# Optimization experiments

Measured on AMD Instinct MI355X. Metric: run time of the kernel, lower is better.

Reference implementation:

```python
import jax, jax.numpy as jnp
import numpy as np

N, E, G = 16384, 65536, 64
IN_F, HID, MID, NCLS = 63, 2048, 1024, 18
EPS = 1e-5
SLOPE = 0.01  # default leaky_relu negative_slope


def setup_inputs() -> dict:
    key = jax.random.key(0)
    ks = jax.random.split(key, 24)
    p = lambda k, shp: jax.random.normal(k, shp, dtype=jnp.float32) * 0.02
    inp = {
        "h": jax.random.normal(ks[0], (N, IN_F), dtype=jnp.float32),
        "src": jax.random.randint(ks[1], (E,), 0, N, dtype=jnp.int32),
        "dst": jax.random.randint(ks[2], (E,), 0, N, dtype=jnp.int32),
        "graph_id": jnp.sort(jax.random.randint(ks[3], (N,), 0, G, dtype=jnp.int32)),
        # SAGEConv layers: fc_self W, fc_neigh W, bias
        "Ws1": p(ks[4], (IN_F, HID)), "Wn1": p(ks[5], (IN_F, HID)), "b1": jnp.zeros((HID,), jnp.float32),
        "Ws2": p(ks[6], (HID, HID)), "Wn2": p(ks[7], (HID, HID)), "b2": jnp.zeros((HID,), jnp.float32),
        "Ws3": p(ks[8], (HID, HID)), "Wn3": p(ks[9], (HID, HID)), "b3": jnp.zeros((HID,), jnp.float32),
        # BatchNorm affine params
        "g1": jnp.ones((HID,), jnp.float32), "be1": jnp.zeros((HID,), jnp.float32),
        "g2": jnp.ones((HID,), jnp.float32), "be2": jnp.zeros((HID,), jnp.float32),
        "g3": jnp.ones((HID,), jnp.float32), "be3": jnp.zeros((HID,), jnp.float32),
        # MLP head
        "fc1_w": p(ks[10], (HID, HID)), "fc1_b": jnp.zeros((HID,), jnp.float32),
        "fc2_w": p(ks[11], (HID, MID)), "fc2_b": jnp.zeros((MID,), jnp.float32),
        "fc3_w": p(ks[12], (MID, NCLS)), "fc3_b": jnp.zeros((NCLS,), jnp.float32),
    }
    return inp


def _sage_mean(h, src, dst, Ws, Wn, b):
    # DGL SAGEConv, aggregator='mean': rst = fc_self(h) + fc_neigh(mean_{u in N(v)} h_u) + bias
    deg = jax.ops.segment_sum(jnp.ones((E,), h.dtype), dst, num_segments=N)
    neigh_sum = jax.ops.segment_sum(h[src], dst, num_segments=N)  # [N, d_in]
    neigh_mean = neigh_sum / jnp.maximum(deg, 1.0)[:, None]       # zero-degree -> 0
    return h @ Ws + neigh_mean @ Wn + b


def _bn(x, gamma, beta):
    # BatchNorm1d in training mode: batch stats over node dim, biased variance
    mu = jnp.mean(x, axis=0)
    var = jnp.mean(jnp.square(x - mu), axis=0)
    return (x - mu) * jax.lax.rsqrt(var + EPS) * gamma + beta


def reference(h, src, dst, graph_id,
              Ws1, Wn1, b1, Ws2, Wn2, b2, Ws3, Wn3, b3,
              g1, be1, g2, be2, g3, be3,
              fc1_w, fc1_b, fc2_w, fc2_b, fc3_w, fc3_b):
    lrelu = lambda x: jax.nn.leaky_relu(x, SLOPE)
    h = lrelu(_bn(_sage_mean(h, src, dst, Ws1, Wn1, b1), g1, be1))
    h = lrelu(_bn(_sage_mean(h, src, dst, Ws2, Wn2, b2), g2, be2))
    h = lrelu(_bn(_sage_mean(h, src, dst, Ws3, Wn3, b3), g3, be3))
    # AvgPooling over batched graph (dropout = identity in eval)
    cnt = jax.ops.segment_sum(jnp.ones((N,), h.dtype), graph_id, num_segments=G)
    hg = jax.ops.segment_sum(h, graph_id, num_segments=G) / jnp.maximum(cnt, 1.0)[:, None]
    x = lrelu(hg @ fc1_w + fc1_b)
    x = lrelu(x @ fc2_w + fc2_b)
    return x @ fc3_w + fc3_b
```

## Files before the change

kernel.cpp:

```cpp
#include <hip/hip_runtime.h>
#include <hip/hip_bf16.h>

#define NN   16384
#define EE   65536
#define GG   64
#define INF  63
#define HID  2048
#define MID  1024
#define NCLS 18
#define EPS  1e-5f
#define SLOPE 0.01f
#define MR   (NN / 128)

typedef unsigned short ushort;
typedef unsigned int uint;

using bf16x8 = __attribute__((ext_vector_type(8))) __bf16;
using f32x4  = __attribute__((ext_vector_type(4))) float;

__device__ __forceinline__ ushort f2us(float x) {
    __hip_bfloat16 b = __float2bfloat16(x);
    return __builtin_bit_cast(ushort, b);
}
__device__ __forceinline__ float us2f(ushort u) {
    return __bfloat162float(__builtin_bit_cast(__hip_bfloat16, u));
}

__device__ __forceinline__ void gll16(const ushort* g, ushort* l) {
    __builtin_amdgcn_global_load_lds(
        (const __attribute__((address_space(1))) uint*)g,
        (__attribute__((address_space(3))) uint*)l, 16, 0, 0);
}


__global__ void k_zero_i(int* __restrict__ p, int n) {
    int i = blockIdx.x * blockDim.x + threadIdx.x;
    if (i < n) p[i] = 0;
}


__global__ void k_count(const int* __restrict__ dst, int* __restrict__ cnt) {
    int e = blockIdx.x * blockDim.x + threadIdx.x;
    if (e < EE) atomicAdd(&cnt[dst[e]], 1);
}

__global__ void k_scan(const int* __restrict__ cnt, int* __restrict__ off,
                       float* __restrict__ deg) {
    __shared__ int sh[1024];
    int t = threadIdx.x;
    int base = t * 16;
    int loc[16];
    int s = 0;
#pragma unroll
    for (int i = 0; i < 16; ++i) {
        int c = cnt[base + i];
        loc[i] = s;
        s += c;
        deg[base + i] = (float)c;
    }
    sh[t] = s;
    __syncthreads();
    for (int d = 1; d < 1024; d <<= 1) {
        int v = (t >= d) ? sh[t - d] : 0;
        __syncthreads();
        sh[t] += v;
        __syncthreads();
    }
    int excl = sh[t] - s;
#pragma unroll
    for (int i = 0; i < 16; ++i) off[base + i] = excl + loc[i];
    if (t == 1023) off[NN] = sh[1023];
}

__global__ void k_fill(const int* __restrict__ src, const int* __restrict__ dst,
                       const int* __restrict__ off, int* __restrict__ cur,
                       int* __restrict__ csr_src) {
    int e = blockIdx.x * blockDim.x + threadIdx.x;
    if (e < EE) {
        int d = dst[e];
        int p = atomicAdd(&cur[d], 1);
        csr_src[off[d] + p] = src[e];
    }
}


__global__ void k_h2bf_c(const float* __restrict__ h, ushort* __restrict__ Xc) {
    int i = blockIdx.x * 256 + threadIdx.x;
    int r = i >> 6, c = i & 63;
    Xc[(size_t)r * 128 + c] = (c < INF) ? f2us(h[(size_t)r * INF + c]) : (ushort)0;
}

__global__ void k_agg_small_c(const float* __restrict__ X, ushort* __restrict__ Xc,
                              const int* __restrict__ off, const int* __restrict__ csr_src,
                              const float* __restrict__ deg) {
    int v = blockIdx.x;
    int f = threadIdx.x;
    float acc = 0.f;
    if (f < INF) {
        int s = off[v], e = off[v + 1];
        for (int i = s; i < e; ++i) acc += X[(size_t)csr_src[i] * INF + f];
        acc /= fmaxf(deg[v], 1.f);
    }
    Xc[(size_t)v * 128 + 64 + f] = f2us(acc);
}


__global__ void k_aggbn(const ushort* __restrict__ Ybf,
                        const float* __restrict__ sc8, const float* __restrict__ sh8,
                        ushort* __restrict__ X, ushort* __restrict__ AggX,
                        const int* __restrict__ off, const int* __restrict__ csr_src,
                        const float* __restrict__ deg) {
    int v = blockIdx.x;
    int t = threadIdx.x;
    int c = t * 8;
    float sc[8], sh[8];
    *(float4*)&sc[0] = *(const float4*)&sc8[c];
    *(float4*)&sc[4] = *(const float4*)&sc8[c + 4];
    *(float4*)&sh[0] = *(const float4*)&sh8[c];
    *(float4*)&sh[4] = *(const float4*)&sh8[c + 4];

    {
        uint4 u = ((const uint4*)(Ybf + (size_t)v * HID))[t];
        uint wds[4] = {u.x, u.y, u.z, u.w};
        uint o[4];
#pragma unroll
        for (int j = 0; j < 4; ++j) {
            float a = sc[2 * j] * us2f((ushort)(wds[j] & 0xffffu)) + sh[2 * j];
            float b = sc[2 * j + 1] * us2f((ushort)(wds[j] >> 16)) + sh[2 * j + 1];
            a = a > 0.f ? a : SLOPE * a;
            b = b > 0.f ? b : SLOPE * b;
            o[j] = (uint)f2us(a) | ((uint)f2us(b) << 16);
        }
        ((uint4*)(X + (size_t)v * HID))[t] = make_uint4(o[0], o[1], o[2], o[3]);
    }

    int s = off[v], e = off[v + 1];
    float acc[8];
#pragma unroll
    for (int j = 0; j < 8; ++j) acc[j] = 0.f;
    for (int i = s; i < e; ++i) {
        uint4 u = ((const uint4*)(Ybf + (size_t)csr_src[i] * HID))[t];
        uint wds[4] = {u.x, u.y, u.z, u.w};
#pragma unroll
        for (int j = 0; j < 4; ++j) {
            float a = sc[2 * j] * us2f((ushort)(wds[j] & 0xffffu)) + sh[2 * j];
            float b = sc[2 * j + 1] * us2f((ushort)(wds[j] >> 16)) + sh[2 * j + 1];
            acc[2 * j]     += a > 0.f ? a : SLOPE * a;
            acc[2 * j + 1] += b > 0.f ? b : SLOPE * b;
        }
    }
    float inv = 1.f / fmaxf(deg[v], 1.f);
    uint o[4];
#pragma unroll
    for (int j = 0; j < 4; ++j)
        o[j] = (uint)f2us(acc[2 * j] * inv) | ((uint)f2us(acc[2 * j + 1] * inv) << 16);
    ((uint4*)(AggX + (size_t)v * HID))[t] = make_uint4(o[0], o[1], o[2], o[3]);
}


__global__ void k_wt2(const float* __restrict__ W0, const float* __restrict__ W1,
                      int K, int N, ushort* __restrict__ Wt0, ushort* __restrict__ Wt1,
                      int Kp) {
    const float* W = blockIdx.z ? W1 : W0;
    ushort* Wt = blockIdx.z ? Wt1 : Wt0;
    __shared__ float t[32][33];
    int kb = blockIdx.y * 32, nb = blockIdx.x * 32;
    int tx = threadIdx.x & 31, ty = threadIdx.x >> 5;
#pragma unroll
    for (int i = 0; i < 32; i += 8) {
        int k = kb + ty + i;
        t[ty + i][tx] = (k < K) ? W[(size_t)k * N + nb + tx] : 0.f;
    }
    __syncthreads();
#pragma unroll
    for (int i = 0; i < 32; i += 8)
        Wt[(size_t)(nb + ty + i) * Kp + kb + tx] = f2us(t[tx][ty + i]);
}

__global__ void k_wt2c(const float* __restrict__ W0, const float* __restrict__ W1,
                       int Kw, int N, ushort* __restrict__ Wtc, int KP) {
    const float* W = blockIdx.z ? W1 : W0;
    const int kOff = blockIdx.z ? (KP / 2) : 0;
    __shared__ float t[32][33];
    int kb = blockIdx.y * 32, nb = blockIdx.x * 32;
    int tx = threadIdx.x & 31, ty = threadIdx.x >> 5;
#pragma unroll
    for (int i = 0; i < 32; i += 8) {
        int k = kb + ty + i;
        t[ty + i][tx] = (k < Kw) ? W[(size_t)k * N + nb + tx] : 0.f;
    }
    __syncthreads();
#pragma unroll
    for (int i = 0; i < 32; i += 8)
        Wtc[(size_t)(nb + ty + i) * KP + kOff + kb + tx] = f2us(t[tx][ty + i]);
}

__global__ void k_wt(const float* __restrict__ W, int K, int N,
                     ushort* __restrict__ Wt, int Kp) {
    __shared__ float t[32][33];
    int kb = blockIdx.y * 32, nb = blockIdx.x * 32;
    int tx = threadIdx.x & 31, ty = threadIdx.x >> 5;
#pragma unroll
    for (int i = 0; i < 32; i += 8) {
        int k = kb + ty + i;
        t[ty + i][tx] = (k < K) ? W[(size_t)k * N + nb + tx] : 0.f;
    }
    __syncthreads();
#pragma unroll
    for (int i = 0; i < 32; i += 8)
        Wt[(size_t)(nb + ty + i) * Kp + kb + tx] = f2us(t[tx][ty + i]);
}


#define BK 64

__global__ __launch_bounds__(256)
void k_mgemm(const ushort* __restrict__ A1, int lda1, const ushort* __restrict__ B1t, int ldb1, int K1,
             const ushort* __restrict__ A2, int lda2, const ushort* __restrict__ B2t, int ldb2, int K2,
             const float* __restrict__ bias, float* __restrict__ Cf, ushort* __restrict__ Cbf,
             int ldc, int fuse_lrelu, float* __restrict__ s1p, float* __restrict__ s2p,
             size_t cStrideZ) {
    __shared__ __align__(16) ushort As[128 * BK];
    __shared__ __align__(16) ushort Bs[128 * BK];
    __shared__ float sb1[4][64];
    __shared__ float sb2[4][64];
    const int tid = threadIdx.x;
    const int lane = tid & 63;
    const int w = tid >> 6;
    const int rowBase = blockIdx.y * 128;
    const int colBase = blockIdx.x * 128;
    const int m0 = (w & 1) * 64;
    const int n0 = (w >> 1) * 64;
    const int z = blockIdx.z;
    A1 += (size_t)z * K1;
    B1t += (size_t)z * K1;
    if (Cf) Cf += (size_t)z * cStrideZ;

    f32x4 acc[4][4];
#pragma unroll
    for (int mi = 0; mi < 4; ++mi)
#pragma unroll
        for (int ni = 0; ni < 4; ++ni) acc[mi][ni] = (f32x4){0.f, 0.f, 0.f, 0.f};

    const int lrow = w * 8 + (lane >> 3);
    const int gc8 = ((lane & 7) ^ (lane >> 3)) * 8;
    const int la = lane & 15, q = lane >> 4;
    const int la7 = lane & 7;

    for (int pass = 0; pass < 2; ++pass) {
        const ushort* A  = pass ? A2 : A1;
        const ushort* Bt = pass ? B2t : B1t;
        const int K   = pass ? K2 : K1;
        const int lda = pass ? lda2 : lda1;
        const int ldb = pass ? ldb2 : ldb1;
        if (A == nullptr) continue;
        const ushort* gA = A + (size_t)(rowBase + lrow) * lda + gc8;
        const ushort* gB = Bt + (size_t)(colBase + lrow) * ldb + gc8;
        for (int kt = 0; kt < K; kt += BK) {
#pragma unroll
            for (int j = 0; j < 4; ++j) {
                gll16(gA + (size_t)(j * 32) * lda + kt, As + j * 2048 + w * 512);
                gll16(gB + (size_t)(j * 32) * ldb + kt, Bs + j * 2048 + w * 512);
            }
            __syncthreads();
#pragma unroll
            for (int kk = 0; kk < 2; ++kk) {
                const int lc8 = ((kk * 4 + q) ^ la7) * 8;
                bf16x8 av[4], bv[4];
#pragma unroll
                for (int mi = 0; mi < 4; ++mi)
                    av[mi] = *(const bf16x8*)&As[(m0 + mi * 16 + la) * BK + lc8];
#pragma unroll
                for (int ni = 0; ni < 4; ++ni)
                    bv[ni] = *(const bf16x8*)&Bs[(n0 + ni * 16 + la) * BK + lc8];
#pragma unroll
                for (int mi = 0; mi < 4; ++mi)
#pragma unroll
                    for (int ni = 0; ni < 4; ++ni)
                        acc[mi][ni] = __builtin_amdgcn_mfma_f32_16x16x32_bf16(
                            av[mi], bv[ni], acc[mi][ni], 0, 0, 0);
            }
            __syncthreads();
        }
    }

#pragma unroll
    for (int mi = 0; mi < 4; ++mi) {
#pragma unroll
        for (int ni = 0; ni < 4; ++ni) {
            const int lc = colBase + n0 + ni * 16 + la;
            const float bv = bias ? bias[lc] : 0.f;
#pragma unroll
            for (int r = 0; r < 4; ++r) {
                const int row = rowBase + m0 + mi * 16 + q * 4 + r;
                float v = acc[mi][ni][r] + bv;
                if (fuse_lrelu) v = v > 0.f ? v : SLOPE * v;
                if (Cbf) Cbf[(size_t)row * ldc + lc] = f2us(v);
                else     Cf[(size_t)row * ldc + lc] = v;
            }
        }
    }

    if (s1p) {
#pragma unroll
        for (int ni = 0; ni < 4; ++ni) {
            const int lc = colBase + n0 + ni * 16 + la;
            const float bv = bias ? bias[lc] : 0.f;
            float t1 = 0.f, t2 = 0.f;
#pragma unroll
            for (int mi = 0; mi < 4; ++mi)
#pragma unroll
                for (int r = 0; r < 4; ++r) {
                    float v = acc[mi][ni][r] + bv;
                    t1 += v;
                    t2 += v * v;
                }
            t1 += __shfl_xor(t1, 16);
            t1 += __shfl_xor(t1, 32);
            t2 += __shfl_xor(t2, 16);
            t2 += __shfl_xor(t2, 32);
            if (q == 0) {
                sb1[w][ni * 16 + la] = t1;
                sb2[w][ni * 16 + la] = t2;
            }
        }
        __syncthreads();
        if (tid < 128) {
            int half = tid >> 6, j = tid & 63;
            float v1 = sb1[2 * half][j] + sb1[2 * half + 1][j];
            float v2 = sb2[2 * half][j] + sb2[2 * half + 1][j];
            size_t o = (size_t)blockIdx.y * ldc + colBase + half * 64 + j;
            s1p[o] = v1;
            s2p[o] = v2;
        }
    }
}


__global__ void k_bn_finalize(const float* __restrict__ p1, const float* __restrict__ p2,
                              const float* __restrict__ gamma, const float* __restrict__ beta,
                              float* __restrict__ scale, float* __restrict__ shift) {
    int c = blockIdx.x * 256 + threadIdx.x;
    if (c >= HID) return;
    float s1 = 0.f, s2 = 0.f;
    for (int rb = 0; rb < MR; ++rb) {
        s1 += p1[(size_t)rb * HID + c];
        s2 += p2[(size_t)rb * HID + c];
    }
    float mean = s1 * (1.f / (float)NN);
    float var = s2 * (1.f / (float)NN) - mean * mean;
    var = fmaxf(var, 0.f);
    float sc = gamma[c] * rsqrtf(var + EPS);
    scale[c] = sc;
    shift[c] = beta[c] - mean * sc;
}


__global__ void k_poolbn(const ushort* __restrict__ Ybf,
                         const float* __restrict__ scale, const float* __restrict__ shift,
                         const int* __restrict__ gstart, ushort* __restrict__ hgbf) {
    int g = blockIdx.y;
    int col = blockIdx.x * 256 + threadIdx.x;
    if (g >= GG) {
        hgbf[(size_t)g * HID + col] = 0;
        return;
    }
    int s = gstart[g], e = gstart[g + 1];
    float sc = scale[col], sh = shift[col];
    float acc = 0.f;
    for (int n = s; n < e; ++n) {
        float v = sc * us2f(Ybf[(size_t)n * HID + col]) + sh;
        acc += v > 0.f ? v : SLOPE * v;
    }
    hgbf[(size_t)g * HID + col] = f2us(acc / fmaxf((float)(e - s), 1.f));
}

__global__ void k_gstart(const int* __restrict__ gid, int* __restrict__ gstart) {
    int g = threadIdx.x;
    if (g > GG) return;
    int lo = 0, hi = NN;
    while (lo < hi) {
        int mid = (lo + hi) >> 1;
        if (gid[mid] < g) lo = mid + 1; else hi = mid;
    }
    gstart[g] = lo;
}


__global__ void k_redhead(const float* __restrict__ part, int P, size_t strideZ,
                          const float* __restrict__ bias, int ldc,
                          ushort* __restrict__ obf, float* __restrict__ of, int n) {
    int i = blockIdx.x * 256 + threadIdx.x;
    if (i >= n) return;
    float s = 0.f;
    for (int p = 0; p < P; ++p) s += part[(size_t)p * strideZ + i];
    s += bias[i % ldc];
    s = s > 0.f ? s : SLOPE * s;
    if (obf) obf[i] = f2us(s);
    else     of[i] = s;
}

__global__ void k_fc3(const float* __restrict__ x2, const float* __restrict__ W,
                      const float* __restrict__ b, float* __restrict__ out) {
    int g = blockIdx.x;
    int tid = threadIdx.x;
    float part[NCLS];
#pragma unroll
    for (int c = 0; c < NCLS; ++c) part[c] = 0.f;
    for (int k = tid; k < MID; k += 256) {
        float x = x2[(size_t)g * MID + k];
        const float* wr = W + (size_t)k * NCLS;
#pragma unroll
        for (int c = 0; c < NCLS; ++c) part[c] += x * wr[c];
    }
    __shared__ float red[4][NCLS];
    int lane = tid & 63, w = tid >> 6;
#pragma unroll
    for (int c = 0; c < NCLS; ++c) {
        float v = part[c];
        for (int o = 32; o > 0; o >>= 1) v += __shfl_down(v, o, 64);
        if (lane == 0) red[w][c] = v;
    }
    __syncthreads();
    if (tid < NCLS)
        out[(size_t)g * NCLS + tid] = red[0][tid] + red[1][tid] + red[2][tid] + red[3][tid] + b[tid];
}


extern "C" void kernel_launch(void* const* d_in, const int* in_sizes, int n_in,
                              void* d_out, int out_size, void* d_ws, size_t ws_size,
                              hipStream_t stream) {
    const float* h        = (const float*)d_in[0];
    const int*   src      = (const int*)d_in[1];
    const int*   dst      = (const int*)d_in[2];
    const int*   graph_id = (const int*)d_in[3];
    const float* Ws1 = (const float*)d_in[4];
    const float* Wn1 = (const float*)d_in[5];
    const float* b1  = (const float*)d_in[6];
    const float* Ws2 = (const float*)d_in[7];
    const float* Wn2 = (const float*)d_in[8];
    const float* b2  = (const float*)d_in[9];
    const float* Ws3 = (const float*)d_in[10];
    const float* Wn3 = (const float*)d_in[11];
    const float* b3  = (const float*)d_in[12];
    const float* g1  = (const float*)d_in[13];
    const float* be1 = (const float*)d_in[14];
    const float* g2  = (const float*)d_in[15];
    const float* be2 = (const float*)d_in[16];
    const float* g3  = (const float*)d_in[17];
    const float* be3 = (const float*)d_in[18];
    const float* fc1_w = (const float*)d_in[19];
    const float* fc1_b = (const float*)d_in[20];
    const float* fc2_w = (const float*)d_in[21];
    const float* fc2_b = (const float*)d_in[22];
    const float* fc3_w = (const float*)d_in[23];
    const float* fc3_b = (const float*)d_in[24];
    float* out = (float*)d_out;

    size_t off_b = 0;
    auto alloc = [&](size_t bytes) -> void* {
        void* p = (char*)d_ws + off_b;
        off_b += (bytes + 255) & ~(size_t)255;
        return p;
    };
    ushort* Wt0    = (ushort*)alloc((size_t)2 * HID * HID * 2);
    ushort* Wt1    = Wt0 + (size_t)HID * HID;
    ushort* X      = (ushort*)alloc((size_t)NN * HID * 2);
    ushort* AggX   = (ushort*)alloc((size_t)NN * HID * 2);
    ushort* Ybf    = (ushort*)alloc((size_t)NN * HID * 2);
    float*  deg    = (float*)alloc((size_t)NN * 4);
    int*    csroff = (int*)alloc((size_t)(NN + 1) * 4);
    int*    cursor = (int*)alloc((size_t)NN * 4);
    int*    csrsrc = (int*)alloc((size_t)EE * 4);
    float*  p1     = (float*)alloc((size_t)MR * HID * 4);
    float*  p2     = (float*)alloc((size_t)MR * HID * 4);
    float*  bnsc   = (float*)alloc((size_t)HID * 4);
    float*  bnsh   = (float*)alloc((size_t)HID * 4);
    int*    gstart = (int*)alloc((size_t)(GG + 1) * 4);

    ushort* Xc128 = X;
    ushort* hgbf  = AggX;
    ushort* x1bf  = AggX + (size_t)128 * HID;
    float*  x2f   = (float*)(AggX + (size_t)2 * 128 * HID);
    float*  partF = (float*)(AggX + (size_t)3 * 128 * HID);

    k_zero_i<<<dim3(NN / 256), dim3(256), 0, stream>>>(cursor, NN);
    k_count<<<dim3(EE / 256), dim3(256), 0, stream>>>(dst, cursor);
    k_scan<<<dim3(1), dim3(1024), 0, stream>>>(cursor, csroff, deg);
    k_zero_i<<<dim3(NN / 256), dim3(256), 0, stream>>>(cursor, NN);
    k_fill<<<dim3(EE / 256), dim3(256), 0, stream>>>(src, dst, csroff, cursor, csrsrc);
    k_gstart<<<dim3(1), dim3(128), 0, stream>>>(graph_id, gstart);

    k_h2bf_c<<<dim3(NN * 64 / 256), dim3(256), 0, stream>>>(h, Xc128);
    k_agg_small_c<<<dim3(NN), dim3(64), 0, stream>>>(h, Xc128, csroff, csrsrc, deg);
    k_wt2c<<<dim3(HID / 32, 2, 2), dim3(256), 0, stream>>>(Ws1, Wn1, INF, HID, Wt0, 128);
    k_mgemm<<<dim3(HID / 128, NN / 128, 1), dim3(256), 0, stream>>>(
        Xc128, 128, Wt0, 128, 128,
        (const ushort*)nullptr, 0, (const ushort*)nullptr, 0, 0,
        b1, (float*)nullptr, Ybf, HID, 0, p1, p2, 0);
    k_bn_finalize<<<dim3(HID / 256), dim3(256), 0, stream>>>(p1, p2, g1, be1, bnsc, bnsh);
    k_aggbn<<<dim3(NN), dim3(256), 0, stream>>>(Ybf, bnsc, bnsh, X, AggX, csroff, csrsrc, deg);

    k_wt2<<<dim3(HID / 32, HID / 32, 2), dim3(256), 0, stream>>>(Ws2, Wn2, HID, HID, Wt0, Wt1, HID);
    k_mgemm<<<dim3(HID / 128, NN / 128, 1), dim3(256), 0, stream>>>(
        X, HID, Wt0, HID, HID,
        AggX, HID, Wt1, HID, HID,
        b2, (float*)nullptr, Ybf, HID, 0, p1, p2, 0);
    k_bn_finalize<<<dim3(HID / 256), dim3(256), 0, stream>>>(p1, p2, g2, be2, bnsc, bnsh);
    k_aggbn<<<dim3(NN), dim3(256), 0, stream>>>(Ybf, bnsc, bnsh, X, AggX, csroff, csrsrc, deg);

    k_wt2<<<dim3(HID / 32, HID / 32, 2), dim3(256), 0, stream>>>(Ws3, Wn3, HID, HID, Wt0, Wt1, HID);
    k_mgemm<<<dim3(HID / 128, NN / 128, 1), dim3(256), 0, stream>>>(
        X, HID, Wt0, HID, HID,
        AggX, HID, Wt1, HID, HID,
        b3, (float*)nullptr, Ybf, HID, 0, p1, p2, 0);
    k_bn_finalize<<<dim3(HID / 256), dim3(256), 0, stream>>>(p1, p2, g3, be3, bnsc, bnsh);

    k_poolbn<<<dim3(HID / 256, 128), dim3(256), 0, stream>>>(Ybf, bnsc, bnsh, gstart, hgbf);

    k_wt<<<dim3(HID / 32, HID / 32), dim3(256), 0, stream>>>(fc1_w, HID, HID, Wt0, HID);
    k_wt<<<dim3(MID / 32, HID / 32), dim3(256), 0, stream>>>(fc2_w, HID, MID, Wt1, HID);
    k_mgemm<<<dim3(HID / 128, 1, 4), dim3(256), 0, stream>>>(
        hgbf, HID, Wt0, HID, HID / 4,
        (const ushort*)nullptr, 0, (const ushort*)nullptr, 0, 0,
        (const float*)nullptr, partF, (ushort*)nullptr, HID, 0,
        (float*)nullptr, (float*)nullptr, (size_t)128 * HID);
    k_redhead<<<dim3(128 * HID / 256), dim3(256), 0, stream>>>(
        partF, 4, (size_t)128 * HID, fc1_b, HID, x1bf, (float*)nullptr, 128 * HID);
    k_mgemm<<<dim3(MID / 128, 1, 4), dim3(256), 0, stream>>>(
        x1bf, HID, Wt1, HID, HID / 4,
        (const ushort*)nullptr, 0, (const ushort*)nullptr, 0, 0,
        (const float*)nullptr, partF, (ushort*)nullptr, MID, 0,
        (float*)nullptr, (float*)nullptr, (size_t)128 * MID);
    k_redhead<<<dim3(128 * MID / 256), dim3(256), 0, stream>>>(
        partF, 4, (size_t)128 * MID, fc2_b, MID, (ushort*)nullptr, x2f, 128 * MID);
    k_fc3<<<dim3(GG), dim3(256), 0, stream>>>(x2f, fc3_w, fc3_b, out);
}
```

Measured before the change: 1.088 ms.

## Add 256x256-tile pipelined MFMA GEMM for the two large SAGE layers

Adds a new GEMM kernel, k_mgemm256, that uses 256x256 output tiles with 512 threads. It double-buffers LDS through direct global-to-LDS loads, interleaves the staging of the next K tile with MFMA phases using barriers and setprio, and swizzles block order for L2 locality. It replaces the 128x128 GEMM for layers 2 and 3 and emits BN partial sums per 256-row block, so bn_finalize now takes the row-block count as a parameter. The aim is more operand reuse per load and better overlap of memory traffic with compute. The cost is higher register and LDS pressure and hand-tuned vmcnt waits that could be fragile.

```diff
diff --git a/kernel.cpp b/kernel.cpp
--- a/kernel.cpp
+++ b/kernel.cpp
@@ -337,13 +337,162 @@
 }
 
 
+#define STAGEH(kti_, wh_) do {                                                 \
+    int _kt = (kti_);                                                          \
+    int _ktc = _kt < KT ? _kt : KT - 1;                                        \
+    int _pass = (_ktc >= kt1);                                                 \
+    int _k0 = (_ktc - (_pass ? kt1 : 0)) << 6;                                 \
+    const ushort* _M;                                                          \
+    int _h, _slot;                                                             \
+    if ((wh_) == 0)      { _M = (_pass ? A2 : A1) + (size_t)rowBase * HID; _h = 0; _slot = 0; } \
+    else if ((wh_) == 2) { _M = (_pass ? A2 : A1) + (size_t)rowBase * HID; _h = 1; _slot = 1; } \
+    else if ((wh_) == 1) { _M = (_pass ? B2t : B1t) + (size_t)colBase * HID; _h = 0; _slot = 2; } \
+    else                 { _M = (_pass ? B2t : B1t) + (size_t)colBase * HID; _h = 1; _slot = 3; } \
+    const ushort* _g = _M + (size_t)(_h * 128 + srow) * HID + (size_t)(_k0 + sch); \
+    ushort* _l = &lds[_kt & 1][_slot][0] + ldsl;                               \
+    gll16(_g, _l);                                                             \
+    gll16(_g + (size_t)64 * HID, _l + 4096);                                   \
+} while (0)
+
+#define PHASE(buf_, hm_, hn_, loadB_, skti_, swh_, wait_) do {                 \
+    const ushort* _Ah = &lds[(buf_)][(hm_)][0];                                \
+    if (loadB_) {                                                              \
+        const ushort* _Bh = &lds[(buf_)][2 + (hn_)][0];                        \
+        _Pragma("unroll")                                                      \
+        for (int g_ = 0; g_ < 2; ++g_) {                                       \
+            b[g_][0] = *(const bf16x8*)&_Bh[brb + g_ * 4096 + c0];             \
+            b[g_][1] = *(const bf16x8*)&_Bh[brb + g_ * 4096 + c1];             \
+        }                                                                      \
+    }                                                                          \
+    _Pragma("unroll")                                                          \
+    for (int f_ = 0; f_ < 4; ++f_) {                                           \
+        a[f_][0] = *(const bf16x8*)&_Ah[arb + f_ * 2048 + c0];                 \
+        a[f_][1] = *(const bf16x8*)&_Ah[arb + f_ * 2048 + c1];                 \
+    }                                                                          \
+    STAGEH((skti_), (swh_));                                                   \
+    __builtin_amdgcn_s_barrier();                                              \
+    __builtin_amdgcn_s_setprio(1);                                             \
+    _Pragma("unroll")                                                          \
+    for (int kk_ = 0; kk_ < 2; ++kk_)                                          \
+        _Pragma("unroll")                                                      \
+        for (int f_ = 0; f_ < 4; ++f_)                                         \
+            _Pragma("unroll")                                                  \
+            for (int g_ = 0; g_ < 2; ++g_)                                     \
+                acc[(hm_) * 4 + f_][(hn_) * 2 + g_] =                          \
+                    __builtin_amdgcn_mfma_f32_16x16x32_bf16(                   \
+                        a[f_][kk_], b[g_][kk_],                                \
+                        acc[(hm_) * 4 + f_][(hn_) * 2 + g_], 0, 0, 0);         \
+    __builtin_amdgcn_s_setprio(0);                                             \
+    if (wait_) asm volatile("s_waitcnt vmcnt(6)" ::: "memory");                \
+    __builtin_amdgcn_s_barrier();                                              \
+} while (0)
+
+__global__ __launch_bounds__(512, 2)
+void k_mgemm256(const ushort* __restrict__ A1, const ushort* __restrict__ B1t,
+                const ushort* __restrict__ A2, const ushort* __restrict__ B2t,
+                int K1, int K2,
+                const float* __restrict__ bias, ushort* __restrict__ Cbf,
+                float* __restrict__ s1p, float* __restrict__ s2p) {
+    __shared__ __align__(16) ushort lds[2][4][128 * 64];
+    __shared__ float sb1[2][256];
+    __shared__ float sb2[2][256];
+
+    const int tid  = threadIdx.x;
+    const int w    = tid >> 6, lane = tid & 63;
+    const int la   = lane & 15, q = lane >> 4, la7 = lane & 7;
+    const int wm   = w >> 2, wn = w & 3;
+
+    const int nx  = gridDim.x;
+    const int lin = blockIdx.y * nx + blockIdx.x;
+    const int cpx = (nx * gridDim.y) >> 3;
+    const int swz = (lin & 7) * cpx + (lin >> 3);
+    const int bx  = swz & (nx - 1), by = swz / nx;
+    const int rowBase = by * 256, colBase = bx * 256;
+
+    const int kt1 = K1 >> 6;
+    const int KT  = kt1 + (K2 >> 6);
+
+    const int srow = tid >> 3;
+    const int sch  = ((tid & 7) ^ (srow & 7)) << 3;
+    const int ldsl = w << 9;
+
+    const int arb = (wm * 16 + la) * 64;
+    const int brb = (wn * 16 + la) * 64;
+    const int c0  = ((0 + q) ^ la7) << 3;
+    const int c1  = ((4 + q) ^ la7) << 3;
+
+    f32x4 acc[8][4];
+#pragma unroll
+    for (int mi = 0; mi < 8; ++mi)
+#pragma unroll
+        for (int ni = 0; ni < 4; ++ni) acc[mi][ni] = (f32x4){0.f, 0.f, 0.f, 0.f};
+    bf16x8 a[4][2], b[2][2];
+
+    STAGEH(0, 0); STAGEH(0, 1); STAGEH(0, 2); STAGEH(0, 3);
+    STAGEH(1, 0);
+    asm volatile("s_waitcnt vmcnt(6)" ::: "memory");
+    __builtin_amdgcn_s_barrier();
+
+    for (int t = 0; t < KT; ++t) {
+        const int bf_ = t & 1;
+        PHASE(bf_, 0, 0, 1, t + 1, 1, 1);
+        PHASE(bf_, 1, 0, 0, t + 1, 2, 1);
+        PHASE(bf_, 0, 1, 1, t + 1, 3, 0);
+        PHASE(bf_, 1, 1, 0, t + 2, 0, 1);
+    }
+
+    __syncthreads();
+
+#pragma unroll
+    for (int mi = 0; mi < 8; ++mi) {
+        const int row = rowBase + (mi >> 2) * 128 + wm * 16 + (mi & 3) * 32 + q * 4;
+#pragma unroll
+        for (int ni = 0; ni < 4; ++ni) {
+            const int col = colBase + (ni >> 1) * 128 + wn * 16 + (ni & 1) * 64 + la;
+            const float bv = bias[col];
+#pragma unroll
+            for (int r = 0; r < 4; ++r) {
+                float v = acc[mi][ni][r] + bv;
+                Cbf[(size_t)(row + r) * HID + col] = f2us(v);
+            }
+        }
+    }
+
+#pragma unroll
+    for (int ni = 0; ni < 4; ++ni) {
+        const int cib = (ni >> 1) * 128 + wn * 16 + (ni & 1) * 64 + la;
+        const float bv = bias[colBase + cib];
+        float t1 = 0.f, t2 = 0.f;
+#pragma unroll
+        for (int mi = 0; mi < 8; ++mi)
+#pragma unroll
+            for (int r = 0; r < 4; ++r) {
+                float v = acc[mi][ni][r] + bv;
+                t1 += v;
+                t2 += v * v;
+            }
+        t1 += __shfl_xor(t1, 16);
+        t1 += __shfl_xor(t1, 32);
+        t2 += __shfl_xor(t2, 16);
+        t2 += __shfl_xor(t2, 32);
+        if (q == 0) { sb1[wm][cib] = t1; sb2[wm][cib] = t2; }
+    }
+    __syncthreads();
+    if (tid < 256) {
+        size_t o = (size_t)by * HID + colBase + tid;
+        s1p[o] = sb1[0][tid] + sb1[1][tid];
+        s2p[o] = sb2[0][tid] + sb2[1][tid];
+    }
+}
+
+
 __global__ void k_bn_finalize(const float* __restrict__ p1, const float* __restrict__ p2,
                               const float* __restrict__ gamma, const float* __restrict__ beta,
-                              float* __restrict__ scale, float* __restrict__ shift) {
+                              float* __restrict__ scale, float* __restrict__ shift, int nrb) {
     int c = blockIdx.x * 256 + threadIdx.x;
     if (c >= HID) return;
     float s1 = 0.f, s2 = 0.f;
-    for (int rb = 0; rb < MR; ++rb) {
+    for (int rb = 0; rb < nrb; ++rb) {
         s1 += p1[(size_t)rb * HID + c];
         s2 += p2[(size_t)rb * HID + c];
     }
@@ -498,23 +647,19 @@
         Xc128, 128, Wt0, 128, 128,
         (const ushort*)nullptr, 0, (const ushort*)nullptr, 0, 0,
         b1, (float*)nullptr, Ybf, HID, 0, p1, p2, 0);
-    k_bn_finalize<<<dim3(HID / 256), dim3(256), 0, stream>>>(p1, p2, g1, be1, bnsc, bnsh);
+    k_bn_finalize<<<dim3(HID / 256), dim3(256), 0, stream>>>(p1, p2, g1, be1, bnsc, bnsh, MR);
     k_aggbn<<<dim3(NN), dim3(256), 0, stream>>>(Ybf, bnsc, bnsh, X, AggX, csroff, csrsrc, deg);
 
     k_wt2<<<dim3(HID / 32, HID / 32, 2), dim3(256), 0, stream>>>(Ws2, Wn2, HID, HID, Wt0, Wt1, HID);
-    k_mgemm<<<dim3(HID / 128, NN / 128, 1), dim3(256), 0, stream>>>(
-        X, HID, Wt0, HID, HID,
-        AggX, HID, Wt1, HID, HID,
-        b2, (float*)nullptr, Ybf, HID, 0, p1, p2, 0);
-    k_bn_finalize<<<dim3(HID / 256), dim3(256), 0, stream>>>(p1, p2, g2, be2, bnsc, bnsh);
+    k_mgemm256<<<dim3(HID / 256, NN / 256), dim3(512), 0, stream>>>(
+        X, Wt0, AggX, Wt1, HID, HID, b2, Ybf, p1, p2);
+    k_bn_finalize<<<dim3(HID / 256), dim3(256), 0, stream>>>(p1, p2, g2, be2, bnsc, bnsh, NN / 256);
     k_aggbn<<<dim3(NN), dim3(256), 0, stream>>>(Ybf, bnsc, bnsh, X, AggX, csroff, csrsrc, deg);
 
     k_wt2<<<dim3(HID / 32, HID / 32, 2), dim3(256), 0, stream>>>(Ws3, Wn3, HID, HID, Wt0, Wt1, HID);
-    k_mgemm<<<dim3(HID / 128, NN / 128, 1), dim3(256), 0, stream>>>(
-        X, HID, Wt0, HID, HID,
-        AggX, HID, Wt1, HID, HID,
-        b3, (float*)nullptr, Ybf, HID, 0, p1, p2, 0);
-    k_bn_finalize<<<dim3(HID / 256), dim3(256), 0, stream>>>(p1, p2, g3, be3, bnsc, bnsh);
+    k_mgemm256<<<dim3(HID / 256, NN / 256), dim3(512), 0, stream>>>(
+        X, Wt0, AggX, Wt1, HID, HID, b3, Ybf, p1, p2);
+    k_bn_finalize<<<dim3(HID / 256), dim3(256), 0, stream>>>(p1, p2, g3, be3, bnsc, bnsh, NN / 256);
 
     k_poolbn<<<dim3(HID / 256, 128), dim3(256), 0, stream>>>(Ybf, bnsc, bnsh, gstart, hgbf);
 
```

Measured after the change: 1.118 ms. 2.7% more time.
